# Kernel tuning notes

Hardware: AMD Instinct MI355X
Metric: run time of the kernel (lower is better)

The kernel has to match this reference:

```python
import jax, jax.numpy as jnp
import numpy as np

SCOPE = 63
IN_CHANNELS = 512
DAMP = 0.12
STD = 8.0


def _mexican_hat(scope, damping, std):
    # Ricker wavelet, centered, shape (1, 1, scope)
    x = jnp.arange(scope, dtype=jnp.float32) - (scope - 1) / 2.0
    norm = damping * (2.0 / (jnp.sqrt(3.0 * std) * np.pi ** 0.25))
    k = norm * (1.0 - (x / std) ** 2) * jnp.exp(-(x ** 2) / (2.0 * std ** 2))
    return k[None, None, :]


def setup_inputs() -> dict:
    key = jax.random.key(0)
    activations = jax.random.normal(key, (32, IN_CHANNELS, 56, 56), dtype=jnp.float32)
    inhibition_filter = _mexican_hat(SCOPE, DAMP, STD)
    return {"activations": activations, "inhibition_filter": inhibition_filter}


def _pad_roll(k, in_channels, scope):
    # zero-pad filter to length in_channels, then roll center to index 0 side
    pad_left = (in_channels - scope) // 2
    pad_right = in_channels - scope - pad_left
    padded = jnp.concatenate(
        [jnp.zeros((pad_left,), k.dtype), k, jnp.zeros((pad_right,), k.dtype)]
    )
    return jnp.roll(padded, in_channels // 2 + 1)


def reference(activations, inhibition_filter):
    C = activations.shape[1]
    kernel = _pad_roll(inhibition_filter[0, 0], C, SCOPE)  # (C,)
    # Circulant Toeplitz matrix: tpl[i] = roll(kernel, i), i.e. tpl[i, j] = kernel[(j - i) % C]
    idx = (jnp.arange(C)[None, :] - jnp.arange(C)[:, None]) % C
    tpl = kernel[idx]  # (C, C)
    # Original: [B, HW, C] @ [C, C] contracting input channel (first tpl axis)
    return jnp.einsum('bchw,cd->bdhw', activations, tpl)
```

## Files before the change

kernel.cpp:

```cpp
#include <hip/hip_runtime.h>
#include <hip/hip_bf16.h>
#include <cstddef>


#define NC    512
#define HW    3136
#define NT    32
#define NTILE (HW / NT)
#define NB    32
#define TPB   256

typedef __attribute__((ext_vector_type(8)))  short bf16x8;
typedef __attribute__((ext_vector_type(4)))  float f32x4;
typedef __attribute__((ext_vector_type(16))) float f32x16;

__device__ __forceinline__ short f2bf(float f) {
    union { __hip_bfloat16 h; short s; } u;
    u.h = __float2bfloat16(f);
    return u.s;
}

__device__ __forceinline__ int swzf(int hw) {
    return (((hw & 7) ^ (hw >> 3)) << 4);
}

__global__ __launch_bounds__(TPB, 5)
void toeplitz_mfma32_kernel(const float* __restrict__ act,
                            const float* __restrict__ filt,
                            float* __restrict__ out) {
    __shared__ __align__(16) unsigned short xs[NT * NC];

    const int tid  = threadIdx.x;
    const int wv   = tid >> 6;
    const int ln   = tid & 63;
    const int bx   = blockIdx.x;
    const int b    = bx / NTILE;
    const int tile = bx - b * NTILE;
    const int hw0  = tile * NT;

    const int r_a = ln & 31;
    const int k0  = (ln >> 5) * 8;
    bf16x8 af[6];
    #pragma unroll
    for (int m = 0; m < 6; ++m) {
        const int delta = 32 - 16 * m;
        #pragma unroll
        for (int i = 0; i < 8; ++i) {
            const int t = delta + 31 + r_a - (k0 + i);
            af[m][i] = (t >= 0 && t < 63) ? f2bf(filt[t]) : (short)0;
        }
    }

    {
        const float* gb = act + (size_t)b * NC * HW + hw0;
        const int g = ln >> 3;
        const int q = ln & 7;
        #pragma unroll
        for (int j = 0; j < 8; ++j) {
            const int r0 = wv * 128 + j * 16 + 2 * g;
            const f32x4 a0 = *reinterpret_cast<const f32x4*>(gb + (size_t)r0 * HW + 4 * q);
            const f32x4 a1 = *reinterpret_cast<const f32x4*>(gb + (size_t)(r0 + 1) * HW + 4 * q);
            #pragma unroll
            for (int t4 = 0; t4 < 4; ++t4) {
                const int hw = 4 * q + t4;
                const unsigned int pk = (unsigned int)(unsigned short)f2bf(a0[t4])
                                      | ((unsigned int)(unsigned short)f2bf(a1[t4]) << 16);
                const int byte = hw * (NC * 2) + ((r0 * 2) ^ swzf(hw));
                *reinterpret_cast<unsigned int*>(reinterpret_cast<char*>(xs) + byte) = pk;
            }
        }
    }
    __syncthreads();

    const int hwl  = ln & 31;
    const int rowbyte = hwl * (NC * 2);
    const int swzv    = swzf(hwl);
    const int kb      = (ln >> 5) * 16;

    #define BFRAG(c0) (*reinterpret_cast<const bf16x8*>(                      \
        reinterpret_cast<const char*>(xs) +                                   \
        (rowbyte + (((((c0) & (NC - 1)) * 2) + kb) ^ swzv))))

    bf16x8 w[12];
    {
        const int cbase = wv * 128 - 32;
        #pragma unroll
        for (int i = 0; i < 12; ++i)
            w[i] = BFRAG(cbase + 16 * i);
    }

    float* ob = out + (size_t)b * NC * HW + hw0 + hwl;
    const int rhalf = (ln >> 5) * 4;

    #pragma unroll
    for (int j = 0; j < 4; ++j) {
        const int d0 = wv * 128 + j * 32;
        f32x16 acc;
        #pragma unroll
        for (int r = 0; r < 16; ++r) acc[r] = 0.0f;
        #pragma unroll
        for (int m = 0; m < 6; ++m)
            acc = __builtin_amdgcn_mfma_f32_32x32x16_bf16(af[m], w[2 * j + m], acc, 0, 0, 0);
        #pragma unroll
        for (int r = 0; r < 16; ++r) {
            const int row = d0 + (r & 3) + 8 * (r >> 2) + rhalf;
            __builtin_nontemporal_store(acc[r], ob + (size_t)row * HW);
        }
    }
    #undef BFRAG
}

extern "C" void kernel_launch(void* const* d_in, const int* in_sizes, int n_in,
                              void* d_out, int out_size, void* d_ws, size_t ws_size,
                              hipStream_t stream) {
    const float* act  = (const float*)d_in[0];
    const float* filt = (const float*)d_in[1];
    float* out = (float*)d_out;
    dim3 grid(NB * NTILE);
    dim3 block(TPB);
    hipLaunchKernelGGL(toeplitz_mfma32_kernel, grid, block, 0, stream,
                       act, filt, out);
}
```

Baseline: 69.13 us.

## Split output channels across two blocks with halo-sized LDS tile

Each block now computes half of the output channels (256) for a 32-pixel tile and loads only the 320 input channels needed, including a circular halo, into shared memory. This doubles the grid and cuts LDS per block, allowing a higher occupancy target (launch bounds raised to 8). The cost is redundant global reads of the 64-channel halo per half (25% more activation loads) and more blocks to schedule.

```diff
diff --git a/kernel.cpp b/kernel.cpp
--- a/kernel.cpp
+++ b/kernel.cpp
@@ -9,6 +9,8 @@
 #define NTILE (HW / NT)
 #define NB    32
 #define TPB   256
+#define CROWS 320
+#define LROW  (CROWS * 2)
 
 typedef __attribute__((ext_vector_type(8)))  short bf16x8;
 typedef __attribute__((ext_vector_type(4)))  float f32x4;
@@ -24,19 +26,22 @@
     return (((hw & 7) ^ (hw >> 3)) << 4);
 }
 
-__global__ __launch_bounds__(TPB, 5)
-void toeplitz_mfma32_kernel(const float* __restrict__ act,
-                            const float* __restrict__ filt,
-                            float* __restrict__ out) {
-    __shared__ __align__(16) unsigned short xs[NT * NC];
+__global__ __launch_bounds__(TPB, 8)
+void toeplitz_half_kernel(const float* __restrict__ act,
+                          const float* __restrict__ filt,
+                          float* __restrict__ out) {
+    __shared__ __align__(16) unsigned short xs[NT * CROWS];
 
     const int tid  = threadIdx.x;
     const int wv   = tid >> 6;
     const int ln   = tid & 63;
     const int bx   = blockIdx.x;
-    const int b    = bx / NTILE;
-    const int tile = bx - b * NTILE;
+    const int ch   = bx & 1;
+    const int rest = bx >> 1;
+    const int b    = rest / NTILE;
+    const int tile = rest - b * NTILE;
     const int hw0  = tile * NT;
+    const int D0   = ch * 256;
 
     const int r_a = ln & 31;
     const int k0  = (ln >> 5) * 8;
@@ -55,9 +60,11 @@
         const float* gb = act + (size_t)b * NC * HW + hw0;
         const int g = ln >> 3;
         const int q = ln & 7;
+        const int GR0 = D0 + 480;
         #pragma unroll
-        for (int j = 0; j < 8; ++j) {
-            const int r0 = wv * 128 + j * 16 + 2 * g;
+        for (int j = 0; j < 5; ++j) {
+            const int cl0 = wv * 80 + j * 16 + 2 * g;
+            const int r0  = (GR0 + cl0) & (NC - 1);
             const f32x4 a0 = *reinterpret_cast<const f32x4*>(gb + (size_t)r0 * HW + 4 * q);
             const f32x4 a1 = *reinterpret_cast<const f32x4*>(gb + (size_t)(r0 + 1) * HW + 4 * q);
             #pragma unroll
@@ -65,36 +72,36 @@
                 const int hw = 4 * q + t4;
                 const unsigned int pk = (unsigned int)(unsigned short)f2bf(a0[t4])
                                       | ((unsigned int)(unsigned short)f2bf(a1[t4]) << 16);
-                const int byte = hw * (NC * 2) + ((r0 * 2) ^ swzf(hw));
+                const int byte = hw * LROW + ((cl0 * 2) ^ swzf(hw));
                 *reinterpret_cast<unsigned int*>(reinterpret_cast<char*>(xs) + byte) = pk;
             }
         }
     }
     __syncthreads();
 
-    const int hwl  = ln & 31;
-    const int rowbyte = hwl * (NC * 2);
+    const int hwl     = ln & 31;
+    const int rowbyte = hwl * LROW;
     const int swzv    = swzf(hwl);
     const int kb      = (ln >> 5) * 16;
 
-    #define BFRAG(c0) (*reinterpret_cast<const bf16x8*>(                      \
-        reinterpret_cast<const char*>(xs) +                                   \
-        (rowbyte + (((((c0) & (NC - 1)) * 2) + kb) ^ swzv))))
-
-    bf16x8 w[12];
+    bf16x8 w[8];
     {
-        const int cbase = wv * 128 - 32;
+        const int clb = wv * 64;
         #pragma unroll
-        for (int i = 0; i < 12; ++i)
-            w[i] = BFRAG(cbase + 16 * i);
+        for (int u = 0; u < 8; ++u) {
+            const int byte = rowbyte + ((((clb + 16 * u) * 2) + kb) ^ swzv);
+            w[u] = *reinterpret_cast<const bf16x8*>(
+                reinterpret_cast<const char*>(xs) + byte);
+        }
     }
 
     float* ob = out + (size_t)b * NC * HW + hw0 + hwl;
     const int rhalf = (ln >> 5) * 4;
+    const int dw    = D0 + wv * 64;
 
     #pragma unroll
-    for (int j = 0; j < 4; ++j) {
-        const int d0 = wv * 128 + j * 32;
+    for (int j = 0; j < 2; ++j) {
+        const int d0 = dw + j * 32;
         f32x16 acc;
         #pragma unroll
         for (int r = 0; r < 16; ++r) acc[r] = 0.0f;
@@ -107,7 +114,6 @@
             __builtin_nontemporal_store(acc[r], ob + (size_t)row * HW);
         }
     }
-    #undef BFRAG
 }
 
 extern "C" void kernel_launch(void* const* d_in, const int* in_sizes, int n_in,
@@ -116,8 +122,8 @@
     const float* act  = (const float*)d_in[0];
     const float* filt = (const float*)d_in[1];
     float* out = (float*)d_out;
-    dim3 grid(NB * NTILE);
+    dim3 grid(NB * NTILE * 2);
     dim3 block(TPB);
-    hipLaunchKernelGGL(toeplitz_mfma32_kernel, grid, block, 0, stream,
+    hipLaunchKernelGGL(toeplitz_half_kernel, grid, block, 0, stream,
                        act, filt, out);
 }
```

Result: slower. 157.3 us (+127.5%).
